# Performance work log

Hardware: AMD Instinct MI355X
Metric: run time of the kernel (lower is better)

## Reference

```python
import jax, jax.numpy as jnp
import numpy as np

RACE_CYCLE = 1024
BET_AMOUNT = 131072
D1, D2 = 64, 16


def setup_inputs() -> dict:
    key = jax.random.key(0)
    ks = jax.random.split(key, 4)
    s1 = 1.0 / np.sqrt(RACE_CYCLE)
    s2 = 1.0 / np.sqrt(D1)
    s3 = 1.0 / np.sqrt(D2)
    return {
        "inputs": jax.random.normal(ks[0], (RACE_CYCLE, BET_AMOUNT), dtype=jnp.float32),
        "W1": jax.random.normal(ks[1], (RACE_CYCLE, D1), dtype=jnp.float32) * s1,
        "b1": jnp.zeros((D1,), dtype=jnp.float32),
        "W2": jax.random.normal(ks[2], (D1, D2), dtype=jnp.float32) * s2,
        "b2": jnp.zeros((D2,), dtype=jnp.float32),
        "W3": jax.random.normal(ks[3], (D2, 1), dtype=jnp.float32) * s3,
        "b3": jnp.zeros((1,), dtype=jnp.float32),
    }


def reference(inputs, W1, b1, W2, b2, W3, b3):
    # tf.map_fn over transposed rows == one batched MLP over inputs.T
    x = inputs.T                                # [bet_amount, race_cycle]
    h1 = jax.nn.relu(x @ W1 + b1)               # [bet_amount, 64]
    h2 = jax.nn.relu(h1 @ W2 + b2)              # [bet_amount, 16]
    out = (h2 @ W3 + b3)[:, 0]                  # [bet_amount]
    return out[None, :]                         # [1, bet_amount]
```

## Files before the change

### kernel.cpp

```cpp
#include <hip/hip_runtime.h>


#define RC 1024
#define BA 131072
#define D1 64
#define D2 16

#define MB 512
#define HS 33

using f16x8  = __attribute__((ext_vector_type(8))) _Float16;
using f32x16 = __attribute__((ext_vector_type(16))) float;

__global__ __launch_bounds__(1024, 4) void mlp3_mfma_v2(
    const float* __restrict__ inputs,
    const float* __restrict__ W1,
    const float* __restrict__ b1,
    const float* __restrict__ W2,
    const float* __restrict__ b2,
    const float* __restrict__ W3,
    const float* __restrict__ b3,
    float* __restrict__ out)
{
    __shared__ __align__(16) _Float16 smem[65536];
    f16x8* Wf = (f16x8*)smem;

    const int t  = threadIdx.x;
    const int l  = t & 63;
    const int wv = t >> 6;

    #pragma unroll
    for (int i = 0; i < 8; ++i) {
        const int lf   = t + i * 1024;
        const int lane = lf & 63;
        const int frag = lf >> 6;
        const int ks   = frag >> 1;
        const int nt   = frag & 1;
        const int n    = (lane & 31) + 32 * nt;
        const int kb   = ks * 16 + (lane >> 5) * 8;
        float w8[8];
        #pragma unroll
        for (int u = 0; u < 8; ++u) w8[u] = W1[(size_t)(kb + u) * D1 + n];
        f16x8 h;
        #pragma unroll
        for (int u = 0; u < 8; ++u) h[u] = (_Float16)w8[u];
        Wf[lf] = h;
    }
    __syncthreads();

    const int    mrow  = blockIdx.x * MB + wv * 32 + (l & 31);
    const size_t kstep = (size_t)16 * BA;
    const float* p0    = inputs + (size_t)((l >> 5) * 8) * BA + mrow;

    f32x16 acc0 = {};
    f32x16 acc1 = {};
    float xa[8], xb[8];

#define LD(X, P) { _Pragma("unroll") \
    for (int u = 0; u < 8; ++u) X[u] = (P)[(size_t)u * BA]; }

#define COMP(X, KS) { \
    f16x8 a; \
    _Pragma("unroll") for (int u = 0; u < 8; ++u) a[u] = (_Float16)X[u]; \
    f16x8 b0f = Wf[(KS) * 128 + l]; \
    f16x8 b1f = Wf[(KS) * 128 + 64 + l]; \
    acc0 = __builtin_amdgcn_mfma_f32_32x32x16_f16(a, b0f, acc0, 0, 0, 0); \
    acc1 = __builtin_amdgcn_mfma_f32_32x32x16_f16(a, b1f, acc1, 0, 0, 0); }

    LD(xa, p0);
    const float* p = p0 + kstep;
    for (int ks = 0; ks < 62; ks += 2) {
        LD(xb, p); p += kstep;
        COMP(xa, ks);
        LD(xa, p); p += kstep;
        COMP(xb, ks + 1);
    }
    LD(xb, p);
    COMP(xa, 62);
    COMP(xb, 63);
#undef LD
#undef COMP

    __syncthreads();
    float* Hw = (float*)smem + wv * (32 * HS);
    const int mc = l & 31;
    const int dh = l >> 5;

    float h2[D2];
    #pragma unroll
    for (int e = 0; e < D2; ++e) h2[e] = (dh == 0) ? b2[e] : 0.f;

#define EPI(ACC, DBASE) { \
    _Pragma("unroll") for (int r = 0; r < 16; ++r) { \
        const int mr = (r & 3) + 8 * (r >> 2) + 4 * dh; \
        Hw[mr * HS + mc] = ACC[r]; \
    } \
    asm volatile("s_waitcnt lgkmcnt(0)" ::: "memory"); \
    _Pragma("unroll") for (int dd = 0; dd < 16; ++dd) { \
        const int d = (DBASE) + dh * 16 + dd; \
        float h = Hw[mc * HS + dh * 16 + dd] + b1[d]; \
        h = h > 0.f ? h : 0.f; \
        _Pragma("unroll") for (int e = 0; e < D2; ++e) \
            h2[e] = fmaf(h, W2[d * D2 + e], h2[e]); \
    } \
    asm volatile("s_waitcnt lgkmcnt(0)" ::: "memory"); }

    EPI(acc0, 0)
    EPI(acc1, 32)
#undef EPI

    #pragma unroll
    for (int e = 0; e < D2; ++e) h2[e] += __shfl_xor(h2[e], 32, 64);

    float o = b3[0];
    #pragma unroll
    for (int e = 0; e < D2; ++e) {
        float h = h2[e] > 0.f ? h2[e] : 0.f;
        o = fmaf(h, W3[e], o);
    }
    if (l < 32)
        out[blockIdx.x * MB + wv * 32 + mc] = o;
}

extern "C" void kernel_launch(void* const* d_in, const int* in_sizes, int n_in,
                              void* d_out, int out_size, void* d_ws, size_t ws_size,
                              hipStream_t stream) {
    const float* inputs = (const float*)d_in[0];
    const float* W1     = (const float*)d_in[1];
    const float* b1     = (const float*)d_in[2];
    const float* W2     = (const float*)d_in[3];
    const float* b2     = (const float*)d_in[4];
    const float* W3     = (const float*)d_in[5];
    const float* b3     = (const float*)d_in[6];
    float* out = (float*)d_out;

    dim3 block(1024);
    dim3 grid(BA / MB);
    mlp3_mfma_v2<<<grid, block, 0, stream>>>(inputs, W1, b1, W2, b2, W3, b3, out);
}
```

Before: 715.5 us.

## Stage input and W1 chunks through double-buffered LDS with float4 loads

Replaces the direct per-lane strided global loads of inputs, and the one-time staging of all of W1 into LDS, with a K-chunked, double-buffered LDS pipeline. Each chunk of 32 rows is fetched with coalesced float4 loads into registers, written to LDS, and read back in MFMA operand layout while the next chunk is being loaded. The block shrinks to 512 threads over 256 columns to cut LDS footprint and raise occupancy. The cost is a barrier per chunk and extra LDS traffic, in exchange for wider coalesced global reads.

```diff
diff --git a/kernel.cpp b/kernel.cpp
--- a/kernel.cpp
+++ b/kernel.cpp
@@ -6,13 +6,15 @@
 #define D1 64
 #define D2 16
 
-#define MB 512
-#define HS 33
+#define MB  256
+#define KC  32
+#define NCH (RC / KC)
+#define HS  33
 
 using f16x8  = __attribute__((ext_vector_type(8))) _Float16;
 using f32x16 = __attribute__((ext_vector_type(16))) float;
 
-__global__ __launch_bounds__(1024, 4) void mlp3_mfma_v2(
+__global__ __launch_bounds__(512, 4) void mlp3_mfma_v3(
     const float* __restrict__ inputs,
     const float* __restrict__ W1,
     const float* __restrict__ b1,
@@ -22,69 +24,88 @@
     const float* __restrict__ b3,
     float* __restrict__ out)
 {
-    __shared__ __align__(16) _Float16 smem[65536];
-    f16x8* Wf = (f16x8*)smem;
+    __shared__ __align__(16) float Ash[2][KC][MB];
+    __shared__ __align__(16) f16x8 Wsh[2][4][64];
 
     const int t  = threadIdx.x;
     const int l  = t & 63;
-    const int wv = t >> 6;
+    const int w  = t >> 6;
+    const int ln = l & 31;
+    const int hi = l >> 5;
+    const int mBase = blockIdx.x * MB;
 
-    #pragma unroll
-    for (int i = 0; i < 8; ++i) {
-        const int lf   = t + i * 1024;
-        const int lane = lf & 63;
-        const int frag = lf >> 6;
-        const int ks   = frag >> 1;
-        const int nt   = frag & 1;
-        const int n    = (lane & 31) + 32 * nt;
-        const int kb   = ks * 16 + (lane >> 5) * 8;
-        float w8[8];
-        #pragma unroll
-        for (int u = 0; u < 8; ++u) w8[u] = W1[(size_t)(kb + u) * D1 + n];
-        f16x8 h;
-        #pragma unroll
-        for (int u = 0; u < 8; ++u) h[u] = (_Float16)w8[u];
-        Wf[lf] = h;
-    }
-    __syncthreads();
+    const int wfrag = t >> 6;
+    const int wks   = t >> 7;
+    const int wnt   = (t >> 6) & 1;
+    const int wlane = t & 63;
+    const int wn    = (wlane & 31) + 32 * wnt;
+    const int wkb   = wks * 16 + (wlane >> 5) * 8;
 
-    const int    mrow  = blockIdx.x * MB + wv * 32 + (l & 31);
-    const size_t kstep = (size_t)16 * BA;
-    const float* p0    = inputs + (size_t)((l >> 5) * 8) * BA + mrow;
+    float4 xr0, xr1, xr2, xr3;
+    float  wr[8];
+
+#define LOADA(c) { \
+    const float* p_ = inputs + (size_t)((c) * KC + w * 4) * BA + (mBase + (l << 2)); \
+    xr0 = *(const float4*)(p_); \
+    xr1 = *(const float4*)(p_ + (size_t)BA); \
+    xr2 = *(const float4*)(p_ + (size_t)2 * BA); \
+    xr3 = *(const float4*)(p_ + (size_t)3 * BA); }
+
+#define LOADW(c) { if (t < 256) { \
+    const float* q_ = W1 + (size_t)((c) * KC + wkb) * D1 + wn; \
+    _Pragma("unroll") for (int u = 0; u < 8; ++u) wr[u] = q_[(size_t)u * D1]; } }
+
+#define WRITE(b) { \
+    { float* d_ = &Ash[b][w * 4][l << 2]; \
+      *(float4*)(d_)          = xr0; \
+      *(float4*)(d_ + MB)     = xr1; \
+      *(float4*)(d_ + 2 * MB) = xr2; \
+      *(float4*)(d_ + 3 * MB) = xr3; } \
+    if (t < 256) { \
+      f16x8 h_; \
+      _Pragma("unroll") for (int u = 0; u < 8; ++u) h_[u] = (_Float16)wr[u]; \
+      Wsh[b][wfrag][wlane] = h_; } }
+
+#define BAR() { asm volatile("s_waitcnt lgkmcnt(0)" ::: "memory"); \
+                __builtin_amdgcn_s_barrier(); \
+                __builtin_amdgcn_sched_barrier(0); }
 
     f32x16 acc0 = {};
     f32x16 acc1 = {};
-    float xa[8], xb[8];
 
-#define LD(X, P) { _Pragma("unroll") \
-    for (int u = 0; u < 8; ++u) X[u] = (P)[(size_t)u * BA]; }
+#define COMPUTE(b) { \
+    _Pragma("unroll") for (int ks = 0; ks < 2; ++ks) { \
+      float av[8]; \
+      _Pragma("unroll") for (int u = 0; u < 8; ++u) \
+        av[u] = Ash[b][ks * 16 + hi * 8 + u][w * 32 + ln]; \
+      f16x8 a_; \
+      _Pragma("unroll") for (int u = 0; u < 8; ++u) a_[u] = (_Float16)av[u]; \
+      f16x8 b0_ = Wsh[b][ks * 2 + 0][l]; \
+      f16x8 b1_ = Wsh[b][ks * 2 + 1][l]; \
+      acc0 = __builtin_amdgcn_mfma_f32_32x32x16_f16(a_, b0_, acc0, 0, 0, 0); \
+      acc1 = __builtin_amdgcn_mfma_f32_32x32x16_f16(a_, b1_, acc1, 0, 0, 0); \
+    } }
 
-#define COMP(X, KS) { \
-    f16x8 a; \
-    _Pragma("unroll") for (int u = 0; u < 8; ++u) a[u] = (_Float16)X[u]; \
-    f16x8 b0f = Wf[(KS) * 128 + l]; \
-    f16x8 b1f = Wf[(KS) * 128 + 64 + l]; \
-    acc0 = __builtin_amdgcn_mfma_f32_32x32x16_f16(a, b0f, acc0, 0, 0, 0); \
-    acc1 = __builtin_amdgcn_mfma_f32_32x32x16_f16(a, b1f, acc1, 0, 0, 0); }
+    LOADA(0); LOADW(0);
+    WRITE(0);
+    LOADA(1); LOADW(1);
+    BAR();
 
-    LD(xa, p0);
-    const float* p = p0 + kstep;
-    for (int ks = 0; ks < 62; ks += 2) {
-        LD(xb, p); p += kstep;
-        COMP(xa, ks);
-        LD(xa, p); p += kstep;
-        COMP(xb, ks + 1);
+    for (int c = 0; c < NCH; ++c) {
+        const int cur = c & 1;
+        if (c + 1 < NCH) { WRITE(cur ^ 1); }
+        if (c + 2 < NCH) { LOADA(c + 2); LOADW(c + 2); }
+        COMPUTE(cur);
+        BAR();
     }
-    LD(xb, p);
-    COMP(xa, 62);
-    COMP(xb, 63);
-#undef LD
-#undef COMP
+#undef LOADA
+#undef LOADW
+#undef WRITE
+#undef COMPUTE
 
-    __syncthreads();
-    float* Hw = (float*)smem + wv * (32 * HS);
-    const int mc = l & 31;
-    const int dh = l >> 5;
+    float* Hw = (float*)Ash + w * (32 * HS);
+    const int mc = ln;
+    const int dh = hi;
 
     float h2[D2];
     #pragma unroll
@@ -96,6 +117,7 @@
         Hw[mr * HS + mc] = ACC[r]; \
     } \
     asm volatile("s_waitcnt lgkmcnt(0)" ::: "memory"); \
+    __builtin_amdgcn_sched_barrier(0); \
     _Pragma("unroll") for (int dd = 0; dd < 16; ++dd) { \
         const int d = (DBASE) + dh * 16 + dd; \
         float h = Hw[mc * HS + dh * 16 + dd] + b1[d]; \
@@ -103,11 +125,13 @@
         _Pragma("unroll") for (int e = 0; e < D2; ++e) \
             h2[e] = fmaf(h, W2[d * D2 + e], h2[e]); \
     } \
-    asm volatile("s_waitcnt lgkmcnt(0)" ::: "memory"); }
+    asm volatile("s_waitcnt lgkmcnt(0)" ::: "memory"); \
+    __builtin_amdgcn_sched_barrier(0); }
 
     EPI(acc0, 0)
     EPI(acc1, 32)
 #undef EPI
+#undef BAR
 
     #pragma unroll
     for (int e = 0; e < D2; ++e) h2[e] += __shfl_xor(h2[e], 32, 64);
@@ -119,7 +143,7 @@
         o = fmaf(h, W3[e], o);
     }
     if (l < 32)
-        out[blockIdx.x * MB + wv * 32 + mc] = o;
+        out[mBase + w * 32 + mc] = o;
 }
 
 extern "C" void kernel_launch(void* const* d_in, const int* in_sizes, int n_in,
@@ -134,7 +158,7 @@
     const float* b3     = (const float*)d_in[6];
     float* out = (float*)d_out;
 
-    dim3 block(1024);
+    dim3 block(512);
     dim3 grid(BA / MB);
-    mlp3_mfma_v2<<<grid, block, 0, stream>>>(inputs, W1, b1, W2, b2, W3, b3, out);
+    mlp3_mfma_v3<<<grid, block, 0, stream>>>(inputs, W1, b1, W2, b2, W3, b3, out);
 }
```

After: 715.5 us. No clear change (-0.0%).
